# Kernel optimization log

Measured on AMD Instinct MI355X. Metric: run time of the kernel, lower is better.

Reference implementation:

```python
import jax, jax.numpy as jnp
import numpy as np

B, S, MW = 128, 256, 21          # batch, sentence length, max word length
VOCAB, E_CHAR, E_WORD, K = 100, 50, 256, 5


def setup_inputs() -> dict:
    key = jax.random.key(0)
    ks = jax.random.split(key, 6)
    padded_sents = jax.random.randint(ks[0], (B, S, MW), 0, VOCAB)
    emb_table = jax.random.normal(ks[1], (VOCAB, E_CHAR), jnp.float32) * 0.1
    emb_table = emb_table.at[0].set(0.0)  # pad_token_idx row zeroed (padding_idx)
    conv_w = jax.random.normal(ks[2], (E_WORD, E_CHAR, K), jnp.float32) * 0.05
    conv_b = jnp.zeros((E_WORD,), jnp.float32)
    w_proj = jax.random.normal(ks[3], (E_WORD, E_WORD), jnp.float32) * 0.05
    b_proj = jnp.zeros((E_WORD,), jnp.float32)
    w_gate = jax.random.normal(ks[4], (E_WORD, E_WORD), jnp.float32) * 0.05
    b_gate = jnp.zeros((E_WORD,), jnp.float32)
    return {
        "padded_sents": padded_sents,
        "emb_table": emb_table,
        "conv_w": conv_w,
        "conv_b": conv_b,
        "w_proj": w_proj,
        "b_proj": b_proj,
        "w_gate": w_gate,
        "b_gate": b_gate,
    }


def reference(padded_sents, emb_table, conv_w, conv_b, w_proj, b_proj, w_gate, b_gate):
    b, s, mw = padded_sents.shape
    # char embedding lookup: [B,S,MW,E_CHAR]
    x = emb_table[padded_sents]
    # fold (B,S) into one batch dim and move channels first: [B*S, E_CHAR, MW]
    x = x.reshape(b * s, mw, -1).transpose(0, 2, 1)
    # Conv1d VALID over char positions: [B*S, E_WORD, MW-K+1]
    y = jax.lax.conv_general_dilated(
        x, conv_w, window_strides=(1,), padding="VALID",
        dimension_numbers=("NCH", "OIH", "NCH"))
    y = jax.nn.relu(y + conv_b[None, :, None])
    # max-pool over remaining char positions: [B*S, E_WORD]
    y = jnp.max(y, axis=2)
    # Highway network
    proj = jax.nn.relu(y @ w_proj.T + b_proj)
    gate = jax.nn.sigmoid(y @ w_gate.T + b_gate)
    out = gate * proj + (1.0 - gate) * y
    # dropout in eval mode (identity)
    return out.reshape(b, s, -1)
```

## Files before the change

kernel.cpp:

```cpp
#include <hip/hip_runtime.h>

#define B_     128
#define S_     256
#define MW_    21
#define VOCAB_ 100
#define EC_    50
#define EW_    256
#define KW_    5
#define T_     17
#define NW_    (B_ * S_)
#define GROWS  (VOCAB_ * KW_)
#define WPB    128
#define GS_STRIDE 72
#define YS_STRIDE 264
#define BS_STRIDE 40

typedef _Float16 f16x8 __attribute__((ext_vector_type(8)));
typedef float    f32x4 __attribute__((ext_vector_type(4)));

__global__ __launch_bounds__(256) void k_prep(const float* __restrict__ emb,
                                              const float* __restrict__ cw,
                                              const float* __restrict__ Wp,
                                              const float* __restrict__ Wg,
                                              _Float16* __restrict__ g,
                                              _Float16* __restrict__ wph,
                                              _Float16* __restrict__ wgh) {
  const int bi = blockIdx.x;
  if (bi < GROWS) {
    __shared__ float es[EC_];
    const int v = bi / KW_;
    const int k = bi % KW_;
    const int o = threadIdx.x;
    if (threadIdx.x < EC_) es[threadIdx.x] = emb[v * EC_ + threadIdx.x];
    __syncthreads();
    float acc = 0.f;
#pragma unroll
    for (int i = 0; i < EC_; ++i)
      acc += es[i] * cw[(o * EC_ + i) * KW_ + k];
    g[bi * EW_ + o] = (_Float16)acc;
  } else {
    const int i = ((bi - GROWS) * 256 + threadIdx.x) * 8;
    const float4 p0 = *(const float4*)&Wp[i], p1 = *(const float4*)&Wp[i + 4];
    const float4 q0 = *(const float4*)&Wg[i], q1 = *(const float4*)&Wg[i + 4];
    f16x8 hp = {(_Float16)p0.x, (_Float16)p0.y, (_Float16)p0.z, (_Float16)p0.w,
                (_Float16)p1.x, (_Float16)p1.y, (_Float16)p1.z, (_Float16)p1.w};
    f16x8 hg = {(_Float16)q0.x, (_Float16)q0.y, (_Float16)q0.z, (_Float16)q0.w,
                (_Float16)q1.x, (_Float16)q1.y, (_Float16)q1.z, (_Float16)q1.w};
    *(f16x8*)&wph[i] = hp;
    *(f16x8*)&wgh[i] = hg;
  }
}

__global__ __launch_bounds__(512, 2) void k_mega(const int* __restrict__ idx,
                                                 const _Float16* __restrict__ g,
                                                 const float* __restrict__ cb,
                                                 const _Float16* __restrict__ wph,
                                                 const _Float16* __restrict__ wgh,
                                                 const float* __restrict__ bp,
                                                 const float* __restrict__ bg,
                                                 float* __restrict__ out) {
  __shared__ __align__(16) _Float16 g_s[GROWS * GS_STRIDE];
  __shared__ __align__(16) _Float16 y_s[WPB * YS_STRIDE];
  const int tid  = threadIdx.x;
  const int wave = tid >> 6, lane = tid & 63;
  const int m0 = blockIdx.x * WPB;

  const int wq = lane >> 3, og = lane & 7;
#pragma unroll
  for (int chunk = 0; chunk < 4; ++chunk) {
    const int oc0 = chunk * 64;
    for (int c = tid; c < GROWS * 8; c += 512) {
      const int row = c >> 3, cc = c & 7;
      *(f16x8*)&g_s[row * GS_STRIDE + cc * 8] =
          *(const f16x8*)&g[row * EW_ + oc0 + cc * 8];
    }
    __syncthreads();

    f16x8 bias;
#pragma unroll
    for (int j = 0; j < 8; ++j) bias[j] = (_Float16)cb[oc0 + og * 8 + j];

#pragma unroll
    for (int it = 0; it < 2; ++it) {
      const int wl = it * 64 + wave * 8 + wq;
      const int* __restrict__ ip = idx + (m0 + wl) * MW_;
      int base[MW_];
#pragma unroll
      for (int c = 0; c < MW_; ++c)
        base[c] = ip[c] * (KW_ * GS_STRIDE) + og * 8;

      f16x8 mx = {0, 0, 0, 0, 0, 0, 0, 0};
#pragma unroll
      for (int t = 0; t < T_; ++t) {
        f16x8 s = bias;
#pragma unroll
        for (int k = 0; k < KW_; ++k)
          s += *(const f16x8*)&g_s[base[t + k] + k * GS_STRIDE];
        mx = __builtin_elementwise_max(mx, s);
      }
      *(f16x8*)&y_s[wl * YS_STRIDE + oc0 + og * 8] = mx;
    }
    __syncthreads();
  }

  _Float16* Bp_s = g_s;
  _Float16* Bg_s = g_s + EW_ * BS_STRIDE;
  const int wm = wave >> 1;
  const int wn = wave & 1;
  const int quad = lane >> 4, r16 = lane & 15;

  f32x4 accp[2][8], accg[2][8];
  const f32x4 zero = {0.f, 0.f, 0.f, 0.f};
#pragma unroll
  for (int mi = 0; mi < 2; ++mi)
#pragma unroll
    for (int nf = 0; nf < 8; ++nf) { accp[mi][nf] = zero; accg[mi][nf] = zero; }

  for (int k0 = 0; k0 < EW_; k0 += 32) {
#pragma unroll
    for (int i2 = 0; i2 < 2; ++i2) {
      const int c2 = i2 * 512 + tid;
      const int r = c2 >> 2, cc = c2 & 3;
      *(f16x8*)&Bp_s[r * BS_STRIDE + cc * 8] = *(const f16x8*)&wph[r * EW_ + k0 + cc * 8];
      *(f16x8*)&Bg_s[r * BS_STRIDE + cc * 8] = *(const f16x8*)&wgh[r * EW_ + k0 + cc * 8];
    }
    __syncthreads();

    f16x8 a[2];
#pragma unroll
    for (int mi = 0; mi < 2; ++mi)
      a[mi] = *(const f16x8*)&y_s[(wm * 32 + mi * 16 + r16) * YS_STRIDE + k0 + quad * 8];

#pragma unroll
    for (int nf = 0; nf < 8; ++nf) {
      const int n = wn * 128 + nf * 16 + r16;
      const f16x8 bpv = *(const f16x8*)&Bp_s[n * BS_STRIDE + quad * 8];
      const f16x8 bgv = *(const f16x8*)&Bg_s[n * BS_STRIDE + quad * 8];
#pragma unroll
      for (int mi = 0; mi < 2; ++mi) {
        accp[mi][nf] = __builtin_amdgcn_mfma_f32_16x16x32_f16(a[mi], bpv, accp[mi][nf], 0, 0, 0);
        accg[mi][nf] = __builtin_amdgcn_mfma_f32_16x16x32_f16(a[mi], bgv, accg[mi][nf], 0, 0, 0);
      }
    }
    __syncthreads();
  }

#pragma unroll
  for (int mi = 0; mi < 2; ++mi)
#pragma unroll
    for (int nf = 0; nf < 8; ++nf) {
      const int n = wn * 128 + nf * 16 + r16;
      const float bpn = bp[n];
      const float bgn = bg[n];
#pragma unroll
      for (int reg = 0; reg < 4; ++reg) {
        const int m = wm * 32 + mi * 16 + quad * 4 + reg;
        float p = fmaxf(accp[mi][nf][reg] + bpn, 0.f);
        const float gz = accg[mi][nf][reg] + bgn;
        const float gate = 1.f / (1.f + __expf(-gz));
        const float yv = (float)y_s[m * YS_STRIDE + n];
        out[(m0 + m) * EW_ + n] = gate * p + (1.f - gate) * yv;
      }
    }
}

extern "C" void kernel_launch(void* const* d_in, const int* in_sizes, int n_in,
                              void* d_out, int out_size, void* d_ws, size_t ws_size,
                              hipStream_t stream) {
  (void)in_sizes; (void)n_in; (void)out_size; (void)ws_size;
  const int*   idx = (const int*)d_in[0];
  const float* emb = (const float*)d_in[1];
  const float* cw  = (const float*)d_in[2];
  const float* cb  = (const float*)d_in[3];
  const float* wp  = (const float*)d_in[4];
  const float* bpp = (const float*)d_in[5];
  const float* wgt = (const float*)d_in[6];
  const float* bgg = (const float*)d_in[7];
  float* out = (float*)d_out;
  _Float16* g_ws = (_Float16*)d_ws;
  _Float16* wp_h = g_ws + GROWS * EW_;
  _Float16* wg_h = wp_h + EW_ * EW_;

  k_prep<<<GROWS + 32, 256, 0, stream>>>(emb, cw, wp, wgt, g_ws, wp_h, wg_h);
  k_mega<<<NW_ / WPB, 512, 0, stream>>>(idx, g_ws, cb, wp_h, wg_h, bpp, bgg, out);
}
```

Measured before the change: 132.0 us.

## Pre-swizzle highway weights and activations into MFMA fragment order, stage weights in halves

The prep kernel now writes the fp16 projection and gate weights in MFMA B-fragment order, so each lane reads its operand with one contiguous 16-byte LDS load. The conv output y is also stored in A-fragment order, and every wave keeps its full K slice of A in registers. The GEMM now stages 64 KB weight halves per matrix instead of 32-wide K tiles, which cuts the number of barriers. The cost is LDS growing to 128 KB per block, which may lower occupancy below two blocks per CU, plus more registers held for the A fragments.

```diff
diff --git a/kernel.cpp b/kernel.cpp
--- a/kernel.cpp
+++ b/kernel.cpp
@@ -11,9 +11,6 @@
 #define NW_    (B_ * S_)
 #define GROWS  (VOCAB_ * KW_)
 #define WPB    128
-#define GS_STRIDE 72
-#define YS_STRIDE 264
-#define BS_STRIDE 40
 
 typedef _Float16 f16x8 __attribute__((ext_vector_type(8)));
 typedef float    f32x4 __attribute__((ext_vector_type(4)));
@@ -23,8 +20,8 @@
                                               const float* __restrict__ Wp,
                                               const float* __restrict__ Wg,
                                               _Float16* __restrict__ g,
-                                              _Float16* __restrict__ wph,
-                                              _Float16* __restrict__ wgh) {
+                                              _Float16* __restrict__ wpf,
+                                              _Float16* __restrict__ wgf) {
   const int bi = blockIdx.x;
   if (bi < GROWS) {
     __shared__ float es[EC_];
@@ -39,28 +36,38 @@
       acc += es[i] * cw[(o * EC_ + i) * KW_ + k];
     g[bi * EW_ + o] = (_Float16)acc;
   } else {
-    const int i = ((bi - GROWS) * 256 + threadIdx.x) * 8;
-    const float4 p0 = *(const float4*)&Wp[i], p1 = *(const float4*)&Wp[i + 4];
-    const float4 q0 = *(const float4*)&Wg[i], q1 = *(const float4*)&Wg[i + 4];
+    const int fl  = (bi - GROWS) * 256 + threadIdx.x;
+    const int nt  = fl >> 9;
+    const int rem = fl & 511;
+    const int ks  = rem >> 6;
+    const int l   = rem & 63;
+    const int n   = nt * 16 + (l & 15);
+    const int kc  = ks * 32 + (l >> 4) * 8;
+    const int src = n * EW_ + kc;
+    const float4 p0 = *(const float4*)&Wp[src], p1 = *(const float4*)&Wp[src + 4];
+    const float4 q0 = *(const float4*)&Wg[src], q1 = *(const float4*)&Wg[src + 4];
     f16x8 hp = {(_Float16)p0.x, (_Float16)p0.y, (_Float16)p0.z, (_Float16)p0.w,
                 (_Float16)p1.x, (_Float16)p1.y, (_Float16)p1.z, (_Float16)p1.w};
     f16x8 hg = {(_Float16)q0.x, (_Float16)q0.y, (_Float16)q0.z, (_Float16)q0.w,
                 (_Float16)q1.x, (_Float16)q1.y, (_Float16)q1.z, (_Float16)q1.w};
-    *(f16x8*)&wph[i] = hp;
-    *(f16x8*)&wgh[i] = hg;
+    *(f16x8*)&wpf[fl * 8] = hp;
+    *(f16x8*)&wgf[fl * 8] = hg;
   }
 }
 
 __global__ __launch_bounds__(512, 2) void k_mega(const int* __restrict__ idx,
                                                  const _Float16* __restrict__ g,
                                                  const float* __restrict__ cb,
-                                                 const _Float16* __restrict__ wph,
-                                                 const _Float16* __restrict__ wgh,
+                                                 const _Float16* __restrict__ wpf,
+                                                 const _Float16* __restrict__ wgf,
                                                  const float* __restrict__ bp,
                                                  const float* __restrict__ bg,
                                                  float* __restrict__ out) {
-  __shared__ __align__(16) _Float16 g_s[GROWS * GS_STRIDE];
-  __shared__ __align__(16) _Float16 y_s[WPB * YS_STRIDE];
+  __shared__ __align__(16) _Float16 lds[65536];
+  _Float16* y_s = lds;
+  _Float16* g_s = lds + 32768;
+  _Float16* B_s = lds + 32768;
+
   const int tid  = threadIdx.x;
   const int wave = tid >> 6, lane = tid & 63;
   const int m0 = blockIdx.x * WPB;
@@ -71,14 +78,16 @@
     const int oc0 = chunk * 64;
     for (int c = tid; c < GROWS * 8; c += 512) {
       const int row = c >> 3, cc = c & 7;
-      *(f16x8*)&g_s[row * GS_STRIDE + cc * 8] =
-          *(const f16x8*)&g[row * EW_ + oc0 + cc * 8];
+      *(f16x8*)&g_s[row * 64 + cc * 8] = *(const f16x8*)&g[row * EW_ + oc0 + cc * 8];
     }
     __syncthreads();
 
     f16x8 bias;
 #pragma unroll
     for (int j = 0; j < 8; ++j) bias[j] = (_Float16)cb[oc0 + og * 8 + j];
+
+    const int ks_w   = chunk * 2 + (og >> 2);
+    const int lane_hi = (og & 3) << 4;
 
 #pragma unroll
     for (int it = 0; it < 2; ++it) {
@@ -87,7 +96,7 @@
       int base[MW_];
 #pragma unroll
       for (int c = 0; c < MW_; ++c)
-        base[c] = ip[c] * (KW_ * GS_STRIDE) + og * 8;
+        base[c] = ip[c] * (KW_ * 64) + og * 8;
 
       f16x8 mx = {0, 0, 0, 0, 0, 0, 0, 0};
 #pragma unroll
@@ -95,73 +104,85 @@
         f16x8 s = bias;
 #pragma unroll
         for (int k = 0; k < KW_; ++k)
-          s += *(const f16x8*)&g_s[base[t + k] + k * GS_STRIDE];
+          s += *(const f16x8*)&g_s[base[t + k] + k * 64];
         mx = __builtin_elementwise_max(mx, s);
       }
-      *(f16x8*)&y_s[wl * YS_STRIDE + oc0 + og * 8] = mx;
+      const int mt = wl >> 4;
+      const int lane_t = (wl & 15) | lane_hi;
+      *(f16x8*)&y_s[((mt * 8 + ks_w) * 64 + lane_t) * 8] = mx;
     }
     __syncthreads();
   }
 
-  _Float16* Bp_s = g_s;
-  _Float16* Bg_s = g_s + EW_ * BS_STRIDE;
-  const int wm = wave >> 1;
-  const int wn = wave & 1;
+  const int mtp = wave >> 1, nh = wave & 1;
   const int quad = lane >> 4, r16 = lane & 15;
 
-  f32x4 accp[2][8], accg[2][8];
+  f16x8 a[2][8];
+#pragma unroll
+  for (int mi = 0; mi < 2; ++mi)
+#pragma unroll
+    for (int ks = 0; ks < 8; ++ks)
+      a[mi][ks] = *(const f16x8*)&y_s[(((mtp * 2 + mi) * 8 + ks) * 64 + lane) * 8];
+
   const f32x4 zero = {0.f, 0.f, 0.f, 0.f};
 #pragma unroll
-  for (int mi = 0; mi < 2; ++mi)
-#pragma unroll
-    for (int nf = 0; nf < 8; ++nf) { accp[mi][nf] = zero; accg[mi][nf] = zero; }
-
-  for (int k0 = 0; k0 < EW_; k0 += 32) {
-#pragma unroll
-    for (int i2 = 0; i2 < 2; ++i2) {
-      const int c2 = i2 * 512 + tid;
-      const int r = c2 >> 2, cc = c2 & 3;
-      *(f16x8*)&Bp_s[r * BS_STRIDE + cc * 8] = *(const f16x8*)&wph[r * EW_ + k0 + cc * 8];
-      *(f16x8*)&Bg_s[r * BS_STRIDE + cc * 8] = *(const f16x8*)&wgh[r * EW_ + k0 + cc * 8];
-    }
-    __syncthreads();
-
-    f16x8 a[2];
+  for (int h = 0; h < 2; ++h) {
+    f32x4 accp[2][4], accg[2][4];
 #pragma unroll
     for (int mi = 0; mi < 2; ++mi)
-      a[mi] = *(const f16x8*)&y_s[(wm * 32 + mi * 16 + r16) * YS_STRIDE + k0 + quad * 8];
-
-#pragma unroll
-    for (int nf = 0; nf < 8; ++nf) {
-      const int n = wn * 128 + nf * 16 + r16;
-      const f16x8 bpv = *(const f16x8*)&Bp_s[n * BS_STRIDE + quad * 8];
-      const f16x8 bgv = *(const f16x8*)&Bg_s[n * BS_STRIDE + quad * 8];
-#pragma unroll
-      for (int mi = 0; mi < 2; ++mi) {
-        accp[mi][nf] = __builtin_amdgcn_mfma_f32_16x16x32_f16(a[mi], bpv, accp[mi][nf], 0, 0, 0);
-        accg[mi][nf] = __builtin_amdgcn_mfma_f32_16x16x32_f16(a[mi], bgv, accg[mi][nf], 0, 0, 0);
+#pragma unroll
+      for (int nf = 0; nf < 4; ++nf) { accp[mi][nf] = zero; accg[mi][nf] = zero; }
+
+#pragma unroll
+    for (int mat = 0; mat < 2; ++mat) {
+      const _Float16* __restrict__ src = (mat == 0 ? wpf : wgf) + h * 32768;
+      for (int c = tid; c < 4096; c += 512)
+        *(f16x8*)&B_s[c * 8] = *(const f16x8*)&src[c * 8];
+      __syncthreads();
+
+#pragma unroll
+      for (int nf = 0; nf < 4; ++nf) {
+        const int ntl = nh * 4 + nf;
+#pragma unroll
+        for (int ks = 0; ks < 8; ++ks) {
+          const f16x8 bv = *(const f16x8*)&B_s[((ntl * 8 + ks) * 64 + lane) * 8];
+          if (mat == 0) {
+#pragma unroll
+            for (int mi = 0; mi < 2; ++mi)
+              accp[mi][nf] = __builtin_amdgcn_mfma_f32_16x16x32_f16(a[mi][ks], bv, accp[mi][nf], 0, 0, 0);
+          } else {
+#pragma unroll
+            for (int mi = 0; mi < 2; ++mi)
+              accg[mi][nf] = __builtin_amdgcn_mfma_f32_16x16x32_f16(a[mi][ks], bv, accg[mi][nf], 0, 0, 0);
+          }
+        }
       }
-    }
-    __syncthreads();
+      __syncthreads();
+    }
+
+#pragma unroll
+    for (int mi = 0; mi < 2; ++mi) {
+      const int mt = mtp * 2 + mi;
+#pragma unroll
+      for (int nf = 0; nf < 4; ++nf) {
+        const int n = h * 128 + nh * 64 + nf * 16 + r16;
+        const float bpn = bp[n];
+        const float bgn = bg[n];
+        const int ks_e = n >> 5;
+        const int lane_e = ((n >> 3) & 3) << 4;
+        const int je = n & 7;
+#pragma unroll
+        for (int reg = 0; reg < 4; ++reg) {
+          const int m = mt * 16 + quad * 4 + reg;
+          float p = fmaxf(accp[mi][nf][reg] + bpn, 0.f);
+          const float gz = accg[mi][nf][reg] + bgn;
+          const float gate = 1.f / (1.f + __expf(-gz));
+          const float yv = (float)y_s[((mt * 8 + ks_e) * 64 + ((m & 15) | lane_e)) * 8 + je];
+          out[(m0 + m) * EW_ + n] = gate * p + (1.f - gate) * yv;
+        }
+      }
+    }
   }
-
-#pragma unroll
-  for (int mi = 0; mi < 2; ++mi)
-#pragma unroll
-    for (int nf = 0; nf < 8; ++nf) {
-      const int n = wn * 128 + nf * 16 + r16;
-      const float bpn = bp[n];
-      const float bgn = bg[n];
-#pragma unroll
-      for (int reg = 0; reg < 4; ++reg) {
-        const int m = wm * 32 + mi * 16 + quad * 4 + reg;
-        float p = fmaxf(accp[mi][nf][reg] + bpn, 0.f);
-        const float gz = accg[mi][nf][reg] + bgn;
-        const float gate = 1.f / (1.f + __expf(-gz));
-        const float yv = (float)y_s[m * YS_STRIDE + n];
-        out[(m0 + m) * EW_ + n] = gate * p + (1.f - gate) * yv;
-      }
-    }
 }
 
 extern "C" void kernel_launch(void* const* d_in, const int* in_sizes, int n_in,
@@ -178,9 +199,9 @@
   const float* bgg = (const float*)d_in[7];
   float* out = (float*)d_out;
   _Float16* g_ws = (_Float16*)d_ws;
-  _Float16* wp_h = g_ws + GROWS * EW_;
-  _Float16* wg_h = wp_h + EW_ * EW_;
-
-  k_prep<<<GROWS + 32, 256, 0, stream>>>(emb, cw, wp, wgt, g_ws, wp_h, wg_h);
-  k_mega<<<NW_ / WPB, 512, 0, stream>>>(idx, g_ws, cb, wp_h, wg_h, bpp, bgg, out);
+  _Float16* wp_f = g_ws + GROWS * EW_;
+  _Float16* wg_f = wp_f + EW_ * EW_;
+
+  k_prep<<<GROWS + 32, 256, 0, stream>>>(emb, cw, wp, wgt, g_ws, wp_f, wg_f);
+  k_mega<<<NW_ / WPB, 512, 0, stream>>>(idx, g_ws, cb, wp_f, wg_f, bpp, bgg, out);
 }
```

Result: no change. 131.4 us (-0.4%).
